# Kernel tuning notes

Hardware: AMD Instinct MI355X
Metric: run time of the kernel (lower is better)

Reference implementation:

```python
import jax, jax.numpy as jnp
import numpy as np

K = 9  # kernel_size (kNN neighbors, includes self since loop=True)


def _knn_edges(x_f, batch, k):
    # x_f: [N, C]. Full pairwise squared distances, masked across batch groups.
    N = x_f.shape[0]
    sq = jnp.sum(x_f * x_f, axis=1)
    d2 = sq[:, None] - 2.0 * (x_f @ x_f.T) + sq[None, :]          # [N, N]
    same = batch[:, None] == batch[None, :]
    d2 = jnp.where(same, d2, jnp.inf)
    neg_d, idx = jax.lax.top_k(-d2, k)                             # k nearest per query row
    valid = jnp.isfinite(neg_d)                                    # guard tiny groups (<k nodes)
    src = idx.reshape(-1)                                          # neighbor -> source
    tgt = jnp.repeat(jnp.arange(N), k)                             # query    -> target
    return src, tgt, valid.reshape(-1)


def _cheb_conv(x_f, src, tgt, valid, W0, W1, bias):
    # ChebConv, K=2, normalization='sym', lambda_max=2.0:
    #   out = x @ W0 + (L_hat x) @ W1 + b,  L_hat = -D^{-1/2} A D^{-1/2} (diag 0)
    N = x_f.shape[0]
    w = jnp.where(valid & (src != tgt), 1.0, 0.0)                  # remove_self_loops
    deg = jax.ops.segment_sum(w, src, num_segments=N)
    dis = jnp.where(deg > 0, jax.lax.rsqrt(jnp.maximum(deg, 1e-30)), 0.0)
    norm = -dis[src] * w * dis[tgt]                                # off-diag of scaled Laplacian
    Tx1 = jax.ops.segment_sum(norm[:, None] * x_f[src], tgt, num_segments=N)
    return x_f @ W0 + Tx1 @ W1 + bias


def setup_inputs() -> dict:
    key = jax.random.key(0)
    k1, k2, k3, k4 = jax.random.split(key, 4)
    B, C, H, W = 8, 192, 32, 32
    Cout = 192
    return {
        "x": jax.random.normal(k1, (B, C, H, W), dtype=jnp.float32),
        "W0": jax.random.normal(k2, (C, Cout), dtype=jnp.float32) * (1.0 / np.sqrt(C)),
        "W1": jax.random.normal(k3, (C, Cout), dtype=jnp.float32) * (1.0 / np.sqrt(C)),
        "bias": jax.random.normal(k4, (Cout,), dtype=jnp.float32) * 0.01,
    }


def reference(x, W0, W1, bias):
    B, C, H, W = x.shape
    N = B * H * W
    x_f = jnp.transpose(x, (0, 2, 3, 1)).reshape(N, C)             # flat_nodes: [B*H*W, C]
    # torch.linspace(0, B, steps=N, dtype=int64) -> truncated float linspace
    batch = jnp.linspace(0.0, float(B), N).astype(jnp.int32)
    src, tgt, valid = _knn_edges(x_f, batch, K)
    return _cheb_conv(x_f, src, tgt, valid, W0, W1, bias)
```

## Files before the change

### kernel.cpp

```cpp
#include <hip/hip_runtime.h>
#include <math.h>

#define NN 8192
#define CF 192
#define KNN 9
#define NSPL 8
#define PKS 12

typedef __bf16 v8bf __attribute__((ext_vector_type(8)));
typedef float f32x16 __attribute__((ext_vector_type(16)));
typedef float f32x4 __attribute__((ext_vector_type(4)));

__device__ __forceinline__ int group_start(int g) {
    int s = (8191 * g + 7) >> 3;
    return s > 8192 ? 8192 : s;
}

__device__ __forceinline__ float disf(int d) {
    return d > 0 ? 1.0f / sqrtf((float)d) : 0.0f;
}

__device__ __forceinline__ unsigned short f2bf(float f) {
    unsigned u = __float_as_uint(f);
    unsigned r = (u + 0x7FFFu + ((u >> 16) & 1u)) >> 16;
    return (unsigned short)r;
}
__device__ __forceinline__ float bf2f(unsigned short h) {
    return __uint_as_float(((unsigned)h) << 16);
}

__global__ __launch_bounds__(256) void transpose_kernel(
    const float* __restrict__ x, unsigned short* __restrict__ xh,
    unsigned short* __restrict__ xl, float* __restrict__ sq,
    int* __restrict__ deg)
{
    __shared__ float tile[32][65];
    int b = blockIdx.x, ht = blockIdx.y;
    int hw0 = ht * 64;
    int tid = threadIdx.x;
    if (tid < 64) deg[(b * 16 + ht) * 64 + tid] = 0;

    float sacc[8];
#pragma unroll
    for (int p = 0; p < 8; ++p) sacc[p] = 0.0f;

    for (int ct = 0; ct < 6; ++ct) {
        int c0 = ct * 32;
        __syncthreads();
#pragma unroll
        for (int p = 0; p < 8; ++p) {
            int c  = p * 4 + (tid >> 6);
            int hw = tid & 63;
            tile[c][hw] = x[(size_t)b * 196608 + (size_t)(c0 + c) * 1024 + hw0 + hw];
        }
        __syncthreads();
#pragma unroll
        for (int p = 0; p < 8; ++p) {
            int hw = p * 8 + (tid >> 5);
            int cc = tid & 31;
            float v = tile[cc][hw];
            size_t o = (size_t)(b * 1024 + hw0 + hw) * CF + c0 + cc;
            unsigned short h = f2bf(v);
            xh[o] = h;
            xl[o] = f2bf(v - bf2f(h));
            sacc[p] = fmaf(v, v, sacc[p]);
        }
    }
#pragma unroll
    for (int p = 0; p < 8; ++p) {
        float s = sacc[p];
#pragma unroll
        for (int off = 16; off > 0; off >>= 1) s += __shfl_xor(s, off, 32);
        if ((tid & 31) == 0)
            sq[(size_t)(b * 1024 + hw0 + p * 8 + (tid >> 5))] = s;
    }
}

__global__ __launch_bounds__(256, 2) void knn_kernel(
    const unsigned short* __restrict__ xh, const unsigned short* __restrict__ xl,
    const float* __restrict__ sq,
    float* __restrict__ pk_d, int* __restrict__ pk_i)
{
    int bid = blockIdx.x;
    int g = bid >> 7;
    int rem = bid & 127;
    int qb = rem >> 3;
    int split = rem & 7;
    int gs = group_start(g);
    int gsize = group_start(g + 1) - gs;
    int q0 = qb * 64;
    int nq = gsize - q0; if (nq > 64) nq = 64;
    if (nq <= 0) return;
    int c0 = split * 128;
    int ncc = gsize - c0; if (ncc > 128) ncc = 128;

    int tid = threadIdx.x;

    if (ncc <= 0) {
        if (tid < nq) {
            int q = gs + q0 + tid;
            size_t base = ((size_t)q * NSPL + split) * PKS;
#pragma unroll
            for (int j = 0; j < KNN; ++j) { pk_d[base + j] = __builtin_inff(); pk_i[base + j] = -1; }
        }
        return;
    }

    __shared__ __align__(16) char smem[34048];
    unsigned short* sm = (unsigned short*)smem;
    __shared__ float sqc_s[128];
    __shared__ float sqq_s[64];

    int lane = tid & 63, w = tid >> 6;
    int arow = (w & 1) * 32 + (lane & 31);
    int k8 = (lane >> 5) * 8;
    int brow0 = (w >> 1) * 64 + (lane & 31);

    if (tid < 64) {
        int qo = q0 + tid; if (qo > gsize - 1) qo = gsize - 1;
        sqq_s[tid] = sq[gs + qo];
    }
    if (tid < 128) {
        sqc_s[tid] = (tid < ncc) ? sq[gs + c0 + tid] : __builtin_inff();
    }

    int rr = tid >> 2, q4 = tid & 3;
    int aq = q0 + rr; if (aq > gsize - 1) aq = gsize - 1;
    int cqA = c0 + rr;      if (cqA > gsize - 1) cqA = gsize - 1;
    int cqB = c0 + 64 + rr; if (cqB > gsize - 1) cqB = gsize - 1;
    int g0 = (gs + aq)  * CF + q4 * 8;
    int g1 = g0 + NN * CF;
    int g2 = (gs + cqA) * CF + q4 * 8;
    int g3 = (gs + cqB) * CF + q4 * 8;
    int g4 = g2 + NN * CF;
    int g5 = g3 + NN * CF;
    int s0 = rr * 40 + q4 * 8;
    int s1 = s0 + 2560;
    int s2 = 5120 + s0;
    int s3 = s2 + 2560;
    int s4 = s2 + 5120;
    int s5 = s3 + 5120;

    f32x16 acc[2];
#pragma unroll
    for (int t = 0; t < 2; ++t)
#pragma unroll
        for (int r = 0; r < 16; ++r) acc[t][r] = 0.0f;

    uint4 d0, d1, d2, d3, d4, d5;
    d0 = *(const uint4*)(xh + g0); d1 = *(const uint4*)(xh + g1);
    d2 = *(const uint4*)(xh + g2); d3 = *(const uint4*)(xh + g3);
    d4 = *(const uint4*)(xh + g4); d5 = *(const uint4*)(xh + g5);

    for (int kb = 0; kb < 6; ++kb) {
        *(uint4*)(sm + s0) = d0; *(uint4*)(sm + s1) = d1;
        *(uint4*)(sm + s2) = d2; *(uint4*)(sm + s3) = d3;
        *(uint4*)(sm + s4) = d4; *(uint4*)(sm + s5) = d5;
        __syncthreads();
        if (kb < 5) {
            int o = (kb + 1) * 32;
            d0 = *(const uint4*)(xh + g0 + o); d1 = *(const uint4*)(xh + g1 + o);
            d2 = *(const uint4*)(xh + g2 + o); d3 = *(const uint4*)(xh + g3 + o);
            d4 = *(const uint4*)(xh + g4 + o); d5 = *(const uint4*)(xh + g5 + o);
        }
#pragma unroll
        for (int h = 0; h < 2; ++h) {
            int ao = arow * 40 + h * 16 + k8;
            v8bf a_hi = *(const v8bf*)(sm + ao);
            v8bf a_lo = *(const v8bf*)(sm + 2560 + ao);
#pragma unroll
            for (int t = 0; t < 2; ++t) {
                int bo = 5120 + (brow0 + t * 32) * 40 + h * 16 + k8;
                v8bf b_hi = *(const v8bf*)(sm + bo);
                v8bf b_lo = *(const v8bf*)(sm + 5120 + bo);
                acc[t] = __builtin_amdgcn_mfma_f32_32x32x16_bf16(a_hi, b_hi, acc[t], 0, 0, 0);
                acc[t] = __builtin_amdgcn_mfma_f32_32x32x16_bf16(a_lo, b_hi, acc[t], 0, 0, 0);
                acc[t] = __builtin_amdgcn_mfma_f32_32x32x16_bf16(a_hi, b_lo, acc[t], 0, 0, 0);
            }
        }
        __syncthreads();
    }

    float (*Ds)[133] = (float(*)[133])smem;
#pragma unroll
    for (int t = 0; t < 2; ++t)
#pragma unroll
        for (int r = 0; r < 16; ++r) {
            int row = (w & 1) * 32 + (r & 3) + 8 * (r >> 2) + 4 * (lane >> 5);
            int col = (w >> 1) * 64 + t * 32 + (lane & 31);
            Ds[row][col] = acc[t][r];
        }
    __syncthreads();

    int sq_ = tid & 63, sch = tid >> 6;
    float sqqv = sqq_s[sq_];
    float pd[KNN]; int pi[KNN];
#pragma unroll
    for (int j = 0; j < KNN; ++j) { pd[j] = __builtin_inff(); pi[j] = -1; }
#pragma unroll
    for (int qt = 0; qt < 4; ++qt) {
        float dv[8], cv[8];
#pragma unroll
        for (int j8 = 0; j8 < 8; ++j8) {
            int c = qt * 32 + sch * 8 + j8;
            dv[j8] = Ds[sq_][c];
            cv[j8] = sqc_s[c];
        }
#pragma unroll
        for (int j8 = 0; j8 < 8; ++j8) {
            float d = (sqqv - 2.0f * dv[j8]) + cv[j8];
            if (d < pd[KNN - 1]) {
                pd[KNN - 1] = d; pi[KNN - 1] = gs + c0 + qt * 32 + sch * 8 + j8;
#pragma unroll
                for (int j = KNN - 1; j > 0; --j) {
                    if (pd[j] < pd[j - 1]) {
                        float tf = pd[j]; pd[j] = pd[j - 1]; pd[j - 1] = tf;
                        int tn = pi[j]; pi[j] = pi[j - 1]; pi[j - 1] = tn;
                    }
                }
            }
        }
    }
    __syncthreads();

    float (*ld)[KNN][65] = (float(*)[KNN][65])smem;
    int   (*li)[KNN][65] = (int(*)[KNN][65])(smem + 9360);
#pragma unroll
    for (int j = 0; j < KNN; ++j) { ld[sch][j][sq_] = pd[j]; li[sch][j][sq_] = pi[j]; }
    __syncthreads();

    if (tid < 64) {
        float dL[4][KNN]; int iL[4][KNN];
#pragma unroll
        for (int ch = 0; ch < 4; ++ch)
#pragma unroll
            for (int j = 0; j < KNN; ++j) {
                dL[ch][j] = ld[ch][j][tid];
                iL[ch][j] = li[ch][j][tid];
            }
        float td[KNN]; int ti[KNN];
#pragma unroll
        for (int j = 0; j < KNN; ++j) { td[j] = __builtin_inff(); ti[j] = -1; }
#pragma unroll
        for (int ch = 0; ch < 4; ++ch) {
#pragma unroll
            for (int j0 = 0; j0 < KNN; ++j0) {
                float d = dL[ch][j0];
                if (!(d < td[KNN - 1])) break;
                td[KNN - 1] = d; ti[KNN - 1] = iL[ch][j0];
#pragma unroll
                for (int j = KNN - 1; j > 0; --j) {
                    if (td[j] < td[j - 1]) {
                        float tf = td[j]; td[j] = td[j - 1]; td[j - 1] = tf;
                        int tn = ti[j]; ti[j] = ti[j - 1]; ti[j - 1] = tn;
                    }
                }
            }
        }
        if (tid < nq) {
            int q = gs + q0 + tid;
            size_t base = ((size_t)q * NSPL + split) * PKS;
#pragma unroll
            for (int j = 0; j < KNN; ++j) { pk_d[base + j] = td[j]; pk_i[base + j] = ti[j]; }
        }
    }
}

__global__ __launch_bounds__(64) void merge_kernel(
    const float* __restrict__ pk_d, const int* __restrict__ pk_i,
    int* __restrict__ edges, int* __restrict__ deg,
    const float* __restrict__ W0, const float* __restrict__ W1,
    unsigned short* __restrict__ wt)
{
    __shared__ float wtile[32][33];
    int tid = threadIdx.x;
    if (blockIdx.x >= 128) {
        int wid = blockIdx.x - 128;
        int mat = wid / 36, rem2 = wid % 36;
        int k0 = (rem2 / 6) * 32, n0 = (rem2 % 6) * 32;
        const float* W = mat ? W1 : W0;
#pragma unroll
        for (int p = 0; p < 4; ++p) {
            int idx = p * 64 + tid;
            int k = idx >> 3, n4 = (idx & 7) * 4;
            *(float4*)&wtile[k][n4] =
                *(const float4*)(W + (size_t)(k0 + k) * CF + n0 + n4);
        }
        __syncthreads();
#pragma unroll
        for (int p = 0; p < 4; ++p) {
            int idx = p * 64 + tid;
            int n = idx >> 3, k4 = (idx & 7) * 4;
            ushort4 h;
            h.x = f2bf(wtile[k4 + 0][n]); h.y = f2bf(wtile[k4 + 1][n]);
            h.z = f2bf(wtile[k4 + 2][n]); h.w = f2bf(wtile[k4 + 3][n]);
            *(ushort4*)(wt + (size_t)mat * 36864 + (size_t)(n0 + n) * CF + k0 + k4) = h;
        }
        return;
    }
    int q = blockIdx.x * 64 + tid;
    float td[KNN]; int ti[KNN];
#pragma unroll
    for (int j = 0; j < KNN; ++j) { td[j] = __builtin_inff(); ti[j] = -1; }
#pragma unroll
    for (int sb = 0; sb < 2; ++sb) {
        float sd[4][KNN]; int si[4][KNN];
#pragma unroll
        for (int s2 = 0; s2 < 4; ++s2) {
            int s = sb * 4 + s2;
            const float* pd = pk_d + ((size_t)q * NSPL + s) * PKS;
            const int*   pp = pk_i + ((size_t)q * NSPL + s) * PKS;
            float4 d0 = *(const float4*)pd;
            float4 d1 = *(const float4*)(pd + 4);
            sd[s2][0] = d0.x; sd[s2][1] = d0.y; sd[s2][2] = d0.z; sd[s2][3] = d0.w;
            sd[s2][4] = d1.x; sd[s2][5] = d1.y; sd[s2][6] = d1.z; sd[s2][7] = d1.w;
            sd[s2][8] = pd[8];
            int4 i0 = *(const int4*)pp;
            int4 i1 = *(const int4*)(pp + 4);
            si[s2][0] = i0.x; si[s2][1] = i0.y; si[s2][2] = i0.z; si[s2][3] = i0.w;
            si[s2][4] = i1.x; si[s2][5] = i1.y; si[s2][6] = i1.z; si[s2][7] = i1.w;
            si[s2][8] = pp[8];
        }
#pragma unroll
        for (int s2 = 0; s2 < 4; ++s2) {
#pragma unroll
            for (int j0 = 0; j0 < KNN; ++j0) {
                float d = sd[s2][j0];
                if (!(d < td[KNN - 1])) break;
                td[KNN - 1] = d; ti[KNN - 1] = si[s2][j0];
#pragma unroll
                for (int j = KNN - 1; j > 0; --j) {
                    if (td[j] < td[j - 1]) {
                        float tf = td[j]; td[j] = td[j - 1]; td[j - 1] = tf;
                        int tn = ti[j]; ti[j] = ti[j - 1]; ti[j - 1] = tn;
                    }
                }
            }
        }
    }
#pragma unroll
    for (int j = 0; j < KNN; ++j) {
        int id = ti[j];
        edges[q * KNN + j] = id;
        if (id >= 0 && id != q) atomicAdd(&deg[id], 1);
    }
}

__global__ __launch_bounds__(256, 2) void out_kernel(
    const unsigned short* __restrict__ xh, const unsigned short* __restrict__ wt,
    const int* __restrict__ edges, const int* __restrict__ deg,
    const float* __restrict__ bias, float* __restrict__ out)
{
    __shared__ __align__(16) unsigned short A0s[16][200];
    __shared__ __align__(16) unsigned short A1s[16][200];
    __shared__ unsigned short Wts[2][CF][32];
    __shared__ float coef_s[16][KNN];
    __shared__ int   nb_s[16][KNN];

    int r0 = blockIdx.x * 16;
    int tid = threadIdx.x;

    for (int t = tid; t < 384; t += 256) {
        int i = t / 24, c8 = (t % 24) * 8;
        *(uint4*)&A0s[i][c8] = *(const uint4*)(xh + (size_t)(r0 + i) * CF + c8);
    }
    if (tid < 16 * KNN) {
        int i = tid / KNN, j = tid % KNN;
        int q = r0 + i;
        int id = edges[q * KNN + j];
        float cf = 0.0f; int s = q;
        if (id >= 0 && id != q) { cf = -disf(deg[id]) * disf(deg[q]); s = id; }
        coef_s[i][j] = cf; nb_s[i][j] = s;
    }
    __syncthreads();
    for (int e = tid; e < 16 * CF / 8; e += 256) {
        int i = e / 24, c8 = (e % 24) * 8;
        float a[8];
#pragma unroll
        for (int j = 0; j < 8; ++j) a[j] = 0.0f;
#pragma unroll
        for (int t = 0; t < KNN; ++t) {
            float cf = coef_s[i][t];
            uint4 v = *(const uint4*)(xh + (size_t)nb_s[i][t] * CF + c8);
            const unsigned short* pv = (const unsigned short*)&v;
#pragma unroll
            for (int j = 0; j < 8; ++j) a[j] = fmaf(cf, bf2f(pv[j]), a[j]);
        }
        uint4 hv;
        hv.x = (unsigned)f2bf(a[0]) | ((unsigned)f2bf(a[1]) << 16);
        hv.y = (unsigned)f2bf(a[2]) | ((unsigned)f2bf(a[3]) << 16);
        hv.z = (unsigned)f2bf(a[4]) | ((unsigned)f2bf(a[5]) << 16);
        hv.w = (unsigned)f2bf(a[6]) | ((unsigned)f2bf(a[7]) << 16);
        *(uint4*)&A1s[i][c8] = hv;
    }

    int lane = tid & 63, w = tid >> 6;
    int m = lane & 15;
    int kq = (lane >> 4) * 8;
    f32x4 acc[3];
#pragma unroll
    for (int t = 0; t < 3; ++t)
#pragma unroll
        for (int r = 0; r < 4; ++r) acc[t][r] = 0.0f;

    for (int kt = 0; kt < 6; ++kt) {
        __syncthreads();
#pragma unroll
        for (int p = 0; p < 6; ++p) {
            int f = p * 256 + tid;
            int mat = f / 768, n = (f % 768) / 4, k16 = (f % 4) * 8;
            *(uint4*)&Wts[mat][n][k16] =
                *(const uint4*)(wt + (size_t)mat * 36864 + (size_t)n * CF + kt * 32 + k16);
        }
        __syncthreads();
        v8bf a0 = *(const v8bf*)&A0s[m][kt * 32 + kq];
        v8bf a1 = *(const v8bf*)&A1s[m][kt * 32 + kq];
#pragma unroll
        for (int t3 = 0; t3 < 3; ++t3) {
            int n0 = w * 48 + t3 * 16;
            v8bf w0 = *(const v8bf*)&Wts[0][n0 + m][kq];
            v8bf w1 = *(const v8bf*)&Wts[1][n0 + m][kq];
            acc[t3] = __builtin_amdgcn_mfma_f32_16x16x32_bf16(a0, w0, acc[t3], 0, 0, 0);
            acc[t3] = __builtin_amdgcn_mfma_f32_16x16x32_bf16(a1, w1, acc[t3], 0, 0, 0);
        }
    }

    int col = lane & 15, rb = (lane >> 4) * 4;
#pragma unroll
    for (int t3 = 0; t3 < 3; ++t3) {
        int n0 = w * 48 + t3 * 16;
        float bv = bias[n0 + col];
#pragma unroll
        for (int r = 0; r < 4; ++r)
            out[(size_t)(r0 + rb + r) * CF + n0 + col] = acc[t3][r] + bv;
    }
}

extern "C" void kernel_launch(void* const* d_in, const int* in_sizes, int n_in,
                              void* d_out, int out_size, void* d_ws, size_t ws_size,
                              hipStream_t stream)
{
    const float* x    = (const float*)d_in[0];
    const float* W0   = (const float*)d_in[1];
    const float* W1   = (const float*)d_in[2];
    const float* bias = (const float*)d_in[3];
    float* out = (float*)d_out;

    char* ws = (char*)d_ws;
    unsigned short* xh = (unsigned short*)ws; ws += (size_t)NN * CF * 2;
    unsigned short* xl = (unsigned short*)ws; ws += (size_t)NN * CF * 2;
    float* sq    = (float*)ws;  ws += (size_t)NN * 4;
    int*   deg   = (int*)ws;    ws += (size_t)NN * 4;
    int*   edges = (int*)ws;    ws += (size_t)NN * KNN * 4;

    unsigned short* wt = xl;

    float* pk_d = out;
    int*   pk_i = (int*)(out + (size_t)NN * NSPL * PKS);

    hipLaunchKernelGGL(transpose_kernel, dim3(8, 16), dim3(256), 0, stream,
                       x, xh, xl, sq, deg);
    hipLaunchKernelGGL(knn_kernel, dim3(1152), dim3(256), 0, stream,
                       xh, xl, sq, pk_d, pk_i);
    hipLaunchKernelGGL(merge_kernel, dim3(200), dim3(64), 0, stream,
                       pk_d, pk_i, edges, deg, W0, W1, wt);
    hipLaunchKernelGGL(out_kernel, dim3(512), dim3(256), 0, stream,
                       xh, wt, edges, deg, bias, out);
}
```

Measured before the change: 121.7 us.

## Halve kNN query tile to 32 rows and raise occupancy to 4 blocks

The kNN distance kernel now handles 32 query rows per block instead of 64, doubling the grid, shrinking shared memory and giving each wave a single 32x32 MFMA accumulator. Launch bounds go from 2 to 4 blocks per CU, so more blocks can be resident and hide the global-load latency. The cost is that candidate tiles are reloaded twice as often, and only half the threads do the top-k selection, so candidate scanning is less parallel per block.

```diff
diff --git a/kernel.cpp b/kernel.cpp
--- a/kernel.cpp
+++ b/kernel.cpp
@@ -76,20 +76,20 @@
     }
 }
 
-__global__ __launch_bounds__(256, 2) void knn_kernel(
+__global__ __launch_bounds__(256, 4) void knn_kernel(
     const unsigned short* __restrict__ xh, const unsigned short* __restrict__ xl,
     const float* __restrict__ sq,
     float* __restrict__ pk_d, int* __restrict__ pk_i)
 {
     int bid = blockIdx.x;
-    int g = bid >> 7;
-    int rem = bid & 127;
+    int g = bid >> 8;
+    int rem = bid & 255;
     int qb = rem >> 3;
     int split = rem & 7;
     int gs = group_start(g);
     int gsize = group_start(g + 1) - gs;
-    int q0 = qb * 64;
-    int nq = gsize - q0; if (nq > 64) nq = 64;
+    int q0 = qb * 32;
+    int nq = gsize - q0; if (nq > 32) nq = 32;
     if (nq <= 0) return;
     int c0 = split * 128;
     int ncc = gsize - c0; if (ncc > 128) ncc = 128;
@@ -106,17 +106,17 @@
         return;
     }
 
-    __shared__ __align__(16) char smem[34048];
+    __shared__ __align__(16) char smem[25600];
     unsigned short* sm = (unsigned short*)smem;
     __shared__ float sqc_s[128];
-    __shared__ float sqq_s[64];
+    __shared__ float sqq_s[32];
 
     int lane = tid & 63, w = tid >> 6;
-    int arow = (w & 1) * 32 + (lane & 31);
+    int arow = lane & 31;
     int k8 = (lane >> 5) * 8;
-    int brow0 = (w >> 1) * 64 + (lane & 31);
-
-    if (tid < 64) {
+    int brow = w * 32 + (lane & 31);
+
+    if (tid < 32) {
         int qo = q0 + tid; if (qo > gsize - 1) qo = gsize - 1;
         sqq_s[tid] = sq[gs + qo];
     }
@@ -124,98 +124,93 @@
         sqc_s[tid] = (tid < ncc) ? sq[gs + c0 + tid] : __builtin_inff();
     }
 
-    int rr = tid >> 2, q4 = tid & 3;
+    int rr = tid >> 3, hl = (tid >> 2) & 1, q4 = tid & 3;
     int aq = q0 + rr; if (aq > gsize - 1) aq = gsize - 1;
-    int cqA = c0 + rr;      if (cqA > gsize - 1) cqA = gsize - 1;
-    int cqB = c0 + 64 + rr; if (cqB > gsize - 1) cqB = gsize - 1;
-    int g0 = (gs + aq)  * CF + q4 * 8;
-    int g1 = g0 + NN * CF;
-    int g2 = (gs + cqA) * CF + q4 * 8;
-    int g3 = (gs + cqB) * CF + q4 * 8;
-    int g4 = g2 + NN * CF;
-    int g5 = g3 + NN * CF;
-    int s0 = rr * 40 + q4 * 8;
-    int s1 = s0 + 2560;
-    int s2 = 5120 + s0;
-    int s3 = s2 + 2560;
-    int s4 = s2 + 5120;
-    int s5 = s3 + 5120;
-
-    f32x16 acc[2];
-#pragma unroll
-    for (int t = 0; t < 2; ++t)
-#pragma unroll
-        for (int r = 0; r < 16; ++r) acc[t][r] = 0.0f;
-
-    uint4 d0, d1, d2, d3, d4, d5;
-    d0 = *(const uint4*)(xh + g0); d1 = *(const uint4*)(xh + g1);
-    d2 = *(const uint4*)(xh + g2); d3 = *(const uint4*)(xh + g3);
-    d4 = *(const uint4*)(xh + g4); d5 = *(const uint4*)(xh + g5);
+    int cq1 = c0 + rr;      if (cq1 > gsize - 1) cq1 = gsize - 1;
+    int cq2 = c0 + 32 + rr; if (cq2 > gsize - 1) cq2 = gsize - 1;
+    int cq3 = c0 + 64 + rr; if (cq3 > gsize - 1) cq3 = gsize - 1;
+    int cq4 = c0 + 96 + rr; if (cq4 > gsize - 1) cq4 = gsize - 1;
+    int hplane = hl * (NN * CF);
+    int ga  = hplane + (gs + aq)  * CF + q4 * 8;
+    int gb1 = hplane + (gs + cq1) * CF + q4 * 8;
+    int gb2 = hplane + (gs + cq2) * CF + q4 * 8;
+    int gb3 = hplane + (gs + cq3) * CF + q4 * 8;
+    int gb4 = hplane + (gs + cq4) * CF + q4 * 8;
+    int sa  = hl * 1280 + rr * 40 + q4 * 8;
+    int sb1 = 2560 + hl * 5120 + rr * 40 + q4 * 8;
+    int sb2 = sb1 + 1280;
+    int sb3 = sb1 + 2560;
+    int sb4 = sb1 + 3840;
+
+    f32x16 acc;
+#pragma unroll
+    for (int r = 0; r < 16; ++r) acc[r] = 0.0f;
+
+    uint4 d0, d1, d2, d3, d4;
+    d0 = *(const uint4*)(xh + ga);
+    d1 = *(const uint4*)(xh + gb1); d2 = *(const uint4*)(xh + gb2);
+    d3 = *(const uint4*)(xh + gb3); d4 = *(const uint4*)(xh + gb4);
 
     for (int kb = 0; kb < 6; ++kb) {
-        *(uint4*)(sm + s0) = d0; *(uint4*)(sm + s1) = d1;
-        *(uint4*)(sm + s2) = d2; *(uint4*)(sm + s3) = d3;
-        *(uint4*)(sm + s4) = d4; *(uint4*)(sm + s5) = d5;
+        *(uint4*)(sm + sa)  = d0;
+        *(uint4*)(sm + sb1) = d1; *(uint4*)(sm + sb2) = d2;
+        *(uint4*)(sm + sb3) = d3; *(uint4*)(sm + sb4) = d4;
         __syncthreads();
         if (kb < 5) {
             int o = (kb + 1) * 32;
-            d0 = *(const uint4*)(xh + g0 + o); d1 = *(const uint4*)(xh + g1 + o);
-            d2 = *(const uint4*)(xh + g2 + o); d3 = *(const uint4*)(xh + g3 + o);
-            d4 = *(const uint4*)(xh + g4 + o); d5 = *(const uint4*)(xh + g5 + o);
+            d0 = *(const uint4*)(xh + ga  + o);
+            d1 = *(const uint4*)(xh + gb1 + o); d2 = *(const uint4*)(xh + gb2 + o);
+            d3 = *(const uint4*)(xh + gb3 + o); d4 = *(const uint4*)(xh + gb4 + o);
         }
 #pragma unroll
         for (int h = 0; h < 2; ++h) {
             int ao = arow * 40 + h * 16 + k8;
             v8bf a_hi = *(const v8bf*)(sm + ao);
-            v8bf a_lo = *(const v8bf*)(sm + 2560 + ao);
-#pragma unroll
-            for (int t = 0; t < 2; ++t) {
-                int bo = 5120 + (brow0 + t * 32) * 40 + h * 16 + k8;
-                v8bf b_hi = *(const v8bf*)(sm + bo);
-                v8bf b_lo = *(const v8bf*)(sm + 5120 + bo);
-                acc[t] = __builtin_amdgcn_mfma_f32_32x32x16_bf16(a_hi, b_hi, acc[t], 0, 0, 0);
-                acc[t] = __builtin_amdgcn_mfma_f32_32x32x16_bf16(a_lo, b_hi, acc[t], 0, 0, 0);
-                acc[t] = __builtin_amdgcn_mfma_f32_32x32x16_bf16(a_hi, b_lo, acc[t], 0, 0, 0);
+            v8bf a_lo = *(const v8bf*)(sm + 1280 + ao);
+            int bo = 2560 + brow * 40 + h * 16 + k8;
+            v8bf b_hi = *(const v8bf*)(sm + bo);
+            v8bf b_lo = *(const v8bf*)(sm + 5120 + bo);
+            acc = __builtin_amdgcn_mfma_f32_32x32x16_bf16(a_hi, b_hi, acc, 0, 0, 0);
+            acc = __builtin_amdgcn_mfma_f32_32x32x16_bf16(a_lo, b_hi, acc, 0, 0, 0);
+            acc = __builtin_amdgcn_mfma_f32_32x32x16_bf16(a_hi, b_lo, acc, 0, 0, 0);
+        }
+        __syncthreads();
+    }
+
+    float (*Ds)[133] = (float(*)[133])smem;
+#pragma unroll
+    for (int r = 0; r < 16; ++r) {
+        int row = (r & 3) + 8 * (r >> 2) + 4 * (lane >> 5);
+        Ds[row][w * 32 + (lane & 31)] = acc[r];
+    }
+    __syncthreads();
+
+    int sq_ = tid & 31, sch = tid >> 5;
+    float pd[KNN]; int pi[KNN];
+#pragma unroll
+    for (int j = 0; j < KNN; ++j) { pd[j] = __builtin_inff(); pi[j] = -1; }
+    if (tid < 128) {
+        float sqqv = sqq_s[sq_];
+#pragma unroll
+        for (int qt = 0; qt < 4; ++qt) {
+            float dv[8], cv[8];
+#pragma unroll
+            for (int j8 = 0; j8 < 8; ++j8) {
+                int c = sch * 32 + qt * 8 + j8;
+                dv[j8] = Ds[sq_][c];
+                cv[j8] = sqc_s[c];
             }
-        }
-        __syncthreads();
-    }
-
-    float (*Ds)[133] = (float(*)[133])smem;
-#pragma unroll
-    for (int t = 0; t < 2; ++t)
-#pragma unroll
-        for (int r = 0; r < 16; ++r) {
-            int row = (w & 1) * 32 + (r & 3) + 8 * (r >> 2) + 4 * (lane >> 5);
-            int col = (w >> 1) * 64 + t * 32 + (lane & 31);
-            Ds[row][col] = acc[t][r];
-        }
-    __syncthreads();
-
-    int sq_ = tid & 63, sch = tid >> 6;
-    float sqqv = sqq_s[sq_];
-    float pd[KNN]; int pi[KNN];
-#pragma unroll
-    for (int j = 0; j < KNN; ++j) { pd[j] = __builtin_inff(); pi[j] = -1; }
-#pragma unroll
-    for (int qt = 0; qt < 4; ++qt) {
-        float dv[8], cv[8];
-#pragma unroll
-        for (int j8 = 0; j8 < 8; ++j8) {
-            int c = qt * 32 + sch * 8 + j8;
-            dv[j8] = Ds[sq_][c];
-            cv[j8] = sqc_s[c];
-        }
-#pragma unroll
-        for (int j8 = 0; j8 < 8; ++j8) {
-            float d = (sqqv - 2.0f * dv[j8]) + cv[j8];
-            if (d < pd[KNN - 1]) {
-                pd[KNN - 1] = d; pi[KNN - 1] = gs + c0 + qt * 32 + sch * 8 + j8;
-#pragma unroll
-                for (int j = KNN - 1; j > 0; --j) {
-                    if (pd[j] < pd[j - 1]) {
-                        float tf = pd[j]; pd[j] = pd[j - 1]; pd[j - 1] = tf;
-                        int tn = pi[j]; pi[j] = pi[j - 1]; pi[j - 1] = tn;
+#pragma unroll
+            for (int j8 = 0; j8 < 8; ++j8) {
+                float d = (sqqv - 2.0f * dv[j8]) + cv[j8];
+                if (d < pd[KNN - 1]) {
+                    pd[KNN - 1] = d; pi[KNN - 1] = gs + c0 + sch * 32 + qt * 8 + j8;
+#pragma unroll
+                    for (int j = KNN - 1; j > 0; --j) {
+                        if (pd[j] < pd[j - 1]) {
+                            float tf = pd[j]; pd[j] = pd[j - 1]; pd[j - 1] = tf;
+                            int tn = pi[j]; pi[j] = pi[j - 1]; pi[j - 1] = tn;
+                        }
                     }
                 }
             }
@@ -223,13 +218,15 @@
     }
     __syncthreads();
 
-    float (*ld)[KNN][65] = (float(*)[KNN][65])smem;
-    int   (*li)[KNN][65] = (int(*)[KNN][65])(smem + 9360);
-#pragma unroll
-    for (int j = 0; j < KNN; ++j) { ld[sch][j][sq_] = pd[j]; li[sch][j][sq_] = pi[j]; }
+    float (*ld)[KNN][33] = (float(*)[KNN][33])smem;
+    int   (*li)[KNN][33] = (int(*)[KNN][33])(smem + 4752);
+    if (tid < 128) {
+#pragma unroll
+        for (int j = 0; j < KNN; ++j) { ld[sch][j][sq_] = pd[j]; li[sch][j][sq_] = pi[j]; }
+    }
     __syncthreads();
 
-    if (tid < 64) {
+    if (tid < 32) {
         float dL[4][KNN]; int iL[4][KNN];
 #pragma unroll
         for (int ch = 0; ch < 4; ++ch)
@@ -460,7 +457,7 @@
 
     hipLaunchKernelGGL(transpose_kernel, dim3(8, 16), dim3(256), 0, stream,
                        x, xh, xl, sq, deg);
-    hipLaunchKernelGGL(knn_kernel, dim3(1152), dim3(256), 0, stream,
+    hipLaunchKernelGGL(knn_kernel, dim3(2304), dim3(256), 0, stream,
                        xh, xl, sq, pk_d, pk_i);
     hipLaunchKernelGGL(merge_kernel, dim3(200), dim3(64), 0, stream,
                        pk_d, pk_i, edges, deg, W0, W1, wt);
```

Measured after the change: 140.5 us. 15.5% more time.

## Double-buffer global prefetch registers and use raw barriers in kNN MFMA loop

Applied to the files above, without the earlier changes.

Restructures the K-loop of the distance GEMM so two K-blocks of global loads are kept in flight in registers (a and b sets), with the loop unrolled by two. It also replaces __syncthreads with an explicit lgkmcnt wait plus s_barrier and sched_barrier, so the compiler does not insert full vmcnt waits that would stall on the outstanding prefetches. The aim is deeper global-load latency hiding, at the cost of extra VGPRs that may reduce occupancy. It also relies on hand-written synchronisation being correct.

```diff
diff --git a/kernel.cpp b/kernel.cpp
--- a/kernel.cpp
+++ b/kernel.cpp
@@ -147,39 +147,68 @@
 #pragma unroll
         for (int r = 0; r < 16; ++r) acc[t][r] = 0.0f;
 
-    uint4 d0, d1, d2, d3, d4, d5;
-    d0 = *(const uint4*)(xh + g0); d1 = *(const uint4*)(xh + g1);
-    d2 = *(const uint4*)(xh + g2); d3 = *(const uint4*)(xh + g3);
-    d4 = *(const uint4*)(xh + g4); d5 = *(const uint4*)(xh + g5);
-
-    for (int kb = 0; kb < 6; ++kb) {
-        *(uint4*)(sm + s0) = d0; *(uint4*)(sm + s1) = d1;
-        *(uint4*)(sm + s2) = d2; *(uint4*)(sm + s3) = d3;
-        *(uint4*)(sm + s4) = d4; *(uint4*)(sm + s5) = d5;
-        __syncthreads();
-        if (kb < 5) {
-            int o = (kb + 1) * 32;
-            d0 = *(const uint4*)(xh + g0 + o); d1 = *(const uint4*)(xh + g1 + o);
-            d2 = *(const uint4*)(xh + g2 + o); d3 = *(const uint4*)(xh + g3 + o);
-            d4 = *(const uint4*)(xh + g4 + o); d5 = *(const uint4*)(xh + g5 + o);
-        }
-#pragma unroll
-        for (int h = 0; h < 2; ++h) {
-            int ao = arow * 40 + h * 16 + k8;
-            v8bf a_hi = *(const v8bf*)(sm + ao);
-            v8bf a_lo = *(const v8bf*)(sm + 2560 + ao);
-#pragma unroll
-            for (int t = 0; t < 2; ++t) {
-                int bo = 5120 + (brow0 + t * 32) * 40 + h * 16 + k8;
-                v8bf b_hi = *(const v8bf*)(sm + bo);
-                v8bf b_lo = *(const v8bf*)(sm + 5120 + bo);
-                acc[t] = __builtin_amdgcn_mfma_f32_32x32x16_bf16(a_hi, b_hi, acc[t], 0, 0, 0);
-                acc[t] = __builtin_amdgcn_mfma_f32_32x32x16_bf16(a_lo, b_hi, acc[t], 0, 0, 0);
-                acc[t] = __builtin_amdgcn_mfma_f32_32x32x16_bf16(a_hi, b_lo, acc[t], 0, 0, 0);
-            }
-        }
-        __syncthreads();
-    }
+    uint4 a0_ = *(const uint4*)(xh + g0);
+    uint4 a1_ = *(const uint4*)(xh + g1);
+    uint4 a2_ = *(const uint4*)(xh + g2);
+    uint4 a3_ = *(const uint4*)(xh + g3);
+    uint4 a4_ = *(const uint4*)(xh + g4);
+    uint4 a5_ = *(const uint4*)(xh + g5);
+    uint4 b0_ = *(const uint4*)(xh + g0 + 32);
+    uint4 b1_ = *(const uint4*)(xh + g1 + 32);
+    uint4 b2_ = *(const uint4*)(xh + g2 + 32);
+    uint4 b3_ = *(const uint4*)(xh + g3 + 32);
+    uint4 b4_ = *(const uint4*)(xh + g4 + 32);
+    uint4 b5_ = *(const uint4*)(xh + g5 + 32);
+
+#define KNN_MFMA_PHASE                                                         \
+    _Pragma("unroll")                                                          \
+    for (int h = 0; h < 2; ++h) {                                              \
+        int ao = arow * 40 + h * 16 + k8;                                      \
+        v8bf a_hi = *(const v8bf*)(sm + ao);                                   \
+        v8bf a_lo = *(const v8bf*)(sm + 2560 + ao);                            \
+        _Pragma("unroll")                                                      \
+        for (int t = 0; t < 2; ++t) {                                          \
+            int bo = 5120 + (brow0 + t * 32) * 40 + h * 16 + k8;               \
+            v8bf b_hi = *(const v8bf*)(sm + bo);                               \
+            v8bf b_lo = *(const v8bf*)(sm + 5120 + bo);                        \
+            acc[t] = __builtin_amdgcn_mfma_f32_32x32x16_bf16(a_hi, b_hi, acc[t], 0, 0, 0); \
+            acc[t] = __builtin_amdgcn_mfma_f32_32x32x16_bf16(a_lo, b_hi, acc[t], 0, 0, 0); \
+            acc[t] = __builtin_amdgcn_mfma_f32_32x32x16_bf16(a_hi, b_lo, acc[t], 0, 0, 0); \
+        }                                                                      \
+    }
+
+#pragma unroll 1
+    for (int kb2 = 0; kb2 < 3; ++kb2) {
+        *(uint4*)(sm + s0) = a0_; *(uint4*)(sm + s1) = a1_;
+        *(uint4*)(sm + s2) = a2_; *(uint4*)(sm + s3) = a3_;
+        *(uint4*)(sm + s4) = a4_; *(uint4*)(sm + s5) = a5_;
+        asm volatile("s_waitcnt lgkmcnt(0)" ::: "memory");
+        __builtin_amdgcn_s_barrier();
+        if (kb2 < 2) {
+            int o = (kb2 + 1) * 64;
+            a0_ = *(const uint4*)(xh + g0 + o); a1_ = *(const uint4*)(xh + g1 + o);
+            a2_ = *(const uint4*)(xh + g2 + o); a3_ = *(const uint4*)(xh + g3 + o);
+            a4_ = *(const uint4*)(xh + g4 + o); a5_ = *(const uint4*)(xh + g5 + o);
+        }
+        KNN_MFMA_PHASE
+        __builtin_amdgcn_s_barrier();
+        __builtin_amdgcn_sched_barrier(0);
+        *(uint4*)(sm + s0) = b0_; *(uint4*)(sm + s1) = b1_;
+        *(uint4*)(sm + s2) = b2_; *(uint4*)(sm + s3) = b3_;
+        *(uint4*)(sm + s4) = b4_; *(uint4*)(sm + s5) = b5_;
+        asm volatile("s_waitcnt lgkmcnt(0)" ::: "memory");
+        __builtin_amdgcn_s_barrier();
+        if (kb2 < 2) {
+            int o = (kb2 + 1) * 64 + 32;
+            b0_ = *(const uint4*)(xh + g0 + o); b1_ = *(const uint4*)(xh + g1 + o);
+            b2_ = *(const uint4*)(xh + g2 + o); b3_ = *(const uint4*)(xh + g3 + o);
+            b4_ = *(const uint4*)(xh + g4 + o); b5_ = *(const uint4*)(xh + g5 + o);
+        }
+        KNN_MFMA_PHASE
+        __builtin_amdgcn_s_barrier();
+        __builtin_amdgcn_sched_barrier(0);
+    }
+#undef KNN_MFMA_PHASE
 
     float (*Ds)[133] = (float(*)[133])smem;
 #pragma unroll
```

Result: slower. 141.1 us (+16.0%).
